# Optimization experiments

Hardware: AMD Instinct MI355X
Metric: run time of the kernel (lower is better)

The kernel has to match this reference:

```python
import jax, jax.numpy as jnp
import numpy as np

N_ENT, N_REL, D, E, NS, B = 100000, 200, 64, 1000000, 4096, 32


def setup_inputs() -> dict:
    key = jax.random.key(0)
    ks = jax.random.split(key, 20)
    s = 1.0 / np.sqrt(D)
    # rotational relation embeddings: [cos|sin ; cos|-sin] -> [2*N_REL, D]
    phases = (2 * np.pi * np.random.RandomState(0).rand(N_REL, D // 2)).astype(np.float32)
    rel = np.concatenate([
        np.concatenate([np.cos(phases), np.sin(phases)], -1),
        np.concatenate([np.cos(phases), -np.sin(phases)], -1)], 0)
    inp = {
        'ent_emb': jax.random.normal(ks[0], (N_ENT, D), jnp.float32) * s,
        'rel_emb': jnp.asarray(rel),
        'gcn_W': jax.random.normal(ks[1], (2, D, D), jnp.float32) * s,
        'gcn_b': jnp.zeros((2, D), jnp.float32),
        'mm_W0': jax.random.normal(ks[2], (3 * D, D), jnp.float32) * s,
        'mm_b0': jnp.zeros((D,), jnp.float32),
        'mm_W1': jax.random.normal(ks[3], (D, D), jnp.float32) * s,
        'mm_b1': jnp.zeros((D,), jnp.float32),
        'mm_Wadv': jax.random.normal(ks[4], (D, 3), jnp.float32) * s,
        'mm_badv': jnp.zeros((3,), jnp.float32),
        'mm_Wval': jax.random.normal(ks[5], (D, 1), jnp.float32) * s,
        'mm_bval': jnp.zeros((1,), jnp.float32),
        'ex_W0': jax.random.normal(ks[6], (D, D), jnp.float32) * s,
        'ex_b0': jnp.zeros((D,), jnp.float32),
        'ex_W1': jax.random.normal(ks[7], (D, D), jnp.float32) * s,
        'ex_b1': jnp.zeros((D,), jnp.float32),
        'ex_Wadv': jax.random.normal(ks[8], (D, 5), jnp.float32) * s,
        'ex_badv': jnp.zeros((5,), jnp.float32),
        'ex_Wval': jax.random.normal(ks[9], (D, 1), jnp.float32) * s,
        'ex_bval': jnp.zeros((1,), jnp.float32),
        'edge_index': jax.random.randint(ks[10], (2, E), 0, N_ENT, jnp.int32),
        'edge_type': jax.random.randint(ks[11], (E,), 0, 2 * N_REL, jnp.int32),
        'short_idx': jax.random.randint(ks[12], (NS,), 0, E, jnp.int32),
        'agent_idx': jax.random.randint(ks[13], (B,), 0, N_ENT, jnp.int32),
    }
    return inp


def _dueling_mlp(h, W0, b0, W1, b1, Wadv, badv, Wval, bval):
    h = jax.nn.relu(h @ W0 + b0)
    h = jax.nn.relu(h @ W1 + b1)
    adv = h @ Wadv + badv
    val = h @ Wval + bval
    return val + adv - adv.mean(-1, keepdims=True)


def reference(ent_emb, rel_emb, gcn_W, gcn_b, mm_W0, mm_b0, mm_W1, mm_b1,
              mm_Wadv, mm_badv, mm_Wval, mm_bval, ex_W0, ex_b0, ex_W1, ex_b1,
              ex_Wadv, ex_badv, ex_Wval, ex_bval,
              edge_index, edge_type, short_idx, agent_idx):
    n = ent_emb.shape[0]
    src, dst = edge_index[0], edge_index[1]
    x = ent_emb
    for l in range(gcn_W.shape[0]):  # GCNConv, normalize=False, no self-loops
        msg = (x @ gcn_W[l])[src]                      # [E, D] gather-transform
        x = jax.ops.segment_sum(msg, dst, num_segments=n) + gcn_b[l]
        x = jax.nn.relu(x)                             # dropout is identity in eval
    # memory-management head: concat(head, relation, tail) for short-term triples
    h_mm = jnp.concatenate([x[src[short_idx]], rel_emb[edge_type[short_idx]],
                            x[dst[short_idx]]], axis=-1)  # [NS, 3D]
    q_mm = _dueling_mlp(h_mm, mm_W0, mm_b0, mm_W1, mm_b1, mm_Wadv, mm_badv, mm_Wval, mm_bval)
    # explore head: agent-node embedding
    q_ex = _dueling_mlp(x[agent_idx], ex_W0, ex_b0, ex_W1, ex_b1, ex_Wadv, ex_badv, ex_Wval, ex_bval)
    return q_mm, q_ex
```

## Files before the change

### kernel.cpp

```cpp
#include <hip/hip_runtime.h>

#define DD 64
#define CAP 32

typedef short bf16x8 __attribute__((ext_vector_type(8)));
typedef float f32x4 __attribute__((ext_vector_type(4)));

static __device__ __forceinline__ unsigned short f2bf(float f) {
  unsigned u = __float_as_uint(f);
  return (unsigned short)((u + 0x7fffu + ((u >> 16) & 1u)) >> 16);
}
static __device__ __forceinline__ unsigned pack2bf(float lo, float hi) {
  return (((unsigned)f2bf(hi)) << 16) | (unsigned)f2bf(lo);
}


__global__ __launch_bounds__(256) void k_zero(
    int* __restrict__ f4, int nf4, int* __restrict__ cnt, int N) {
  const int i = blockIdx.x * 256 + threadIdx.x;
  if (i < nf4) f4[i] = 0;
  if (i < N) cnt[i] = 0;
}

__global__ __launch_bounds__(256) void k_flag2(
    const int* __restrict__ sidx, const int* __restrict__ src,
    const int* __restrict__ dst, const int* __restrict__ aidx,
    unsigned char* __restrict__ flags, int NS, int B) {
  const int i = blockIdx.x * 256 + threadIdx.x;
  if (i < NS) {
    int e = sidx[i];
    flags[src[e]] = 1;
    flags[dst[e]] = 1;
  } else if (i < NS + B) {
    flags[aidx[i - NS]] = 1;
  }
}

__global__ __launch_bounds__(256) void k_flagA(
    const int* __restrict__ src, const int* __restrict__ dst,
    unsigned char* __restrict__ flags, int E) {
  const int e = blockIdx.x * 256 + threadIdx.x;
  if (e < E && (flags[dst[e]] & 1)) {
    int s = src[e];
    flags[s] = flags[s] | 2;
  }
}

__device__ __forceinline__ void gemm_body(
    const float* __restrict__ x, const float* __restrict__ W,
    unsigned short* __restrict__ yh, int N, int bid, int nB) {
  __shared__ unsigned short wt[DD * DD];
  __shared__ float ys[4][16][68];
  for (int i = threadIdx.x; i < DD * DD; i += 256) {
    int k = i >> 6, n = i & 63;
    wt[n * DD + k] = f2bf(W[i]);
  }
  __syncthreads();
  const int wave = threadIdx.x >> 6;
  const int lane = threadIdx.x & 63;
  const int g = lane >> 4;
  const int m = lane & 15;
  bf16x8 bfr[8];
#pragma unroll
  for (int nt = 0; nt < 4; ++nt)
#pragma unroll
    for (int m2 = 0; m2 < 2; ++m2) {
      const int base = (nt * 16 + m) * DD + 4 * g + 32 * m2;
      ushort4 lo = *(const ushort4*)&wt[base];
      ushort4 hi = *(const ushort4*)&wt[base + 16];
      bf16x8 f;
      f[0] = (short)lo.x; f[1] = (short)lo.y; f[2] = (short)lo.z; f[3] = (short)lo.w;
      f[4] = (short)hi.x; f[5] = (short)hi.y; f[6] = (short)hi.z; f[7] = (short)hi.w;
      bfr[nt * 2 + m2] = f;
    }
  const int tiles = (N + 15) / 16;
  for (int t = bid * 4 + wave; t < tiles; t += nB * 4) {
    const int row = t * 16 + m;
    const int rsafe = (row < N) ? row : (N - 1);
    const float* xr = x + (size_t)rsafe * DD + 4 * g;
    float4 a0 = *(const float4*)(xr + 0);
    float4 a1 = *(const float4*)(xr + 16);
    float4 a2 = *(const float4*)(xr + 32);
    float4 a3 = *(const float4*)(xr + 48);
    bf16x8 af0, af1;
    af0[0] = (short)f2bf(a0.x); af0[1] = (short)f2bf(a0.y);
    af0[2] = (short)f2bf(a0.z); af0[3] = (short)f2bf(a0.w);
    af0[4] = (short)f2bf(a1.x); af0[5] = (short)f2bf(a1.y);
    af0[6] = (short)f2bf(a1.z); af0[7] = (short)f2bf(a1.w);
    af1[0] = (short)f2bf(a2.x); af1[1] = (short)f2bf(a2.y);
    af1[2] = (short)f2bf(a2.z); af1[3] = (short)f2bf(a2.w);
    af1[4] = (short)f2bf(a3.x); af1[5] = (short)f2bf(a3.y);
    af1[6] = (short)f2bf(a3.z); af1[7] = (short)f2bf(a3.w);
    f32x4 acc0 = {0.f, 0.f, 0.f, 0.f}, acc1 = acc0, acc2 = acc0, acc3 = acc0;
    acc0 = __builtin_amdgcn_mfma_f32_16x16x32_bf16(af0, bfr[0], acc0, 0, 0, 0);
    acc0 = __builtin_amdgcn_mfma_f32_16x16x32_bf16(af1, bfr[1], acc0, 0, 0, 0);
    acc1 = __builtin_amdgcn_mfma_f32_16x16x32_bf16(af0, bfr[2], acc1, 0, 0, 0);
    acc1 = __builtin_amdgcn_mfma_f32_16x16x32_bf16(af1, bfr[3], acc1, 0, 0, 0);
    acc2 = __builtin_amdgcn_mfma_f32_16x16x32_bf16(af0, bfr[4], acc2, 0, 0, 0);
    acc2 = __builtin_amdgcn_mfma_f32_16x16x32_bf16(af1, bfr[5], acc2, 0, 0, 0);
    acc3 = __builtin_amdgcn_mfma_f32_16x16x32_bf16(af0, bfr[6], acc3, 0, 0, 0);
    acc3 = __builtin_amdgcn_mfma_f32_16x16x32_bf16(af1, bfr[7], acc3, 0, 0, 0);
#pragma unroll
    for (int r = 0; r < 4; ++r) {
      ys[wave][4 * g + r][0 * 16 + m] = acc0[r];
      ys[wave][4 * g + r][1 * 16 + m] = acc1[r];
      ys[wave][4 * g + r][2 * 16 + m] = acc2[r];
      ys[wave][4 * g + r][3 * 16 + m] = acc3[r];
    }
    if (row < N) {
      unsigned short* yr = yh + (size_t)row * DD + g * 16;
      const float* s = &ys[wave][m][g * 16];
      uint4 olo, ohi;
      olo.x = pack2bf(s[0], s[1]);
      olo.y = pack2bf(s[2], s[3]);
      olo.z = pack2bf(s[4], s[5]);
      olo.w = pack2bf(s[6], s[7]);
      ohi.x = pack2bf(s[8], s[9]);
      ohi.y = pack2bf(s[10], s[11]);
      ohi.z = pack2bf(s[12], s[13]);
      ohi.w = pack2bf(s[14], s[15]);
      *(uint4*)yr = olo;
      *(uint4*)(yr + 8) = ohi;
    }
  }
}

__global__ __launch_bounds__(256) void k_pregf(
    const float* __restrict__ x, const float* __restrict__ W,
    unsigned short* __restrict__ yh, int N, int GB,
    const int* __restrict__ src, const int* __restrict__ dst,
    const unsigned char* __restrict__ flags, int* __restrict__ cnt,
    int* __restrict__ csr, int E) {
  const int bid = blockIdx.x;
  if (bid < GB) {
    gemm_body(x, W, yh, N, bid, GB);
  } else {
    int e = (bid - GB) * 256 + threadIdx.x;
    if (e < E) {
      int d = dst[e];
      if (flags[d]) {
        int slot = atomicAdd(&cnt[d], 1);
        if (slot < CAP) csr[d * CAP + slot] = src[e];
      }
    }
  }
}

__global__ __launch_bounds__(256) void k_gemm(
    const float* __restrict__ x, const float* __restrict__ W,
    unsigned short* __restrict__ yh, int N) {
  gemm_body(x, W, yh, N, blockIdx.x, gridDim.x);
}

__global__ __launch_bounds__(256) void k_gather_h(
    const unsigned short* __restrict__ yh, const int* __restrict__ cnt,
    const int* __restrict__ csr, const float* __restrict__ b,
    float* __restrict__ outp, int N, const unsigned char* __restrict__ flags,
    int bit) {
  const int wave = threadIdx.x >> 6;
  const int lane = threadIdx.x & 63;
  const int h = lane >> 5;
  const int c = lane & 31;
  const int n = blockIdx.x * 4 + wave;
  if (n >= N) return;
  if (!(flags[n] & bit)) return;
  const float b0r = b[2 * c];
  const float b1r = b[2 * c + 1];
  int i = n * CAP;
  int c2 = cnt[n];
  c2 = (c2 < CAP) ? c2 : CAP;
  const int end = i + c2;
  float a0 = 0.f, a1 = 0.f;
  for (; i + 8 <= end; i += 8) {
    int ib = __builtin_amdgcn_readfirstlane(i);
    int sA = csr[ib + 0 + h];
    int sB = csr[ib + 2 + h];
    int sC = csr[ib + 4 + h];
    int sD = csr[ib + 6 + h];
    unsigned vA = *(const unsigned*)&yh[(size_t)sA * DD + 2 * c];
    unsigned vB = *(const unsigned*)&yh[(size_t)sB * DD + 2 * c];
    unsigned vC = *(const unsigned*)&yh[(size_t)sC * DD + 2 * c];
    unsigned vD = *(const unsigned*)&yh[(size_t)sD * DD + 2 * c];
    a0 += (__uint_as_float(vA << 16) + __uint_as_float(vB << 16)) +
          (__uint_as_float(vC << 16) + __uint_as_float(vD << 16));
    a1 += (__uint_as_float(vA & 0xffff0000u) + __uint_as_float(vB & 0xffff0000u)) +
          (__uint_as_float(vC & 0xffff0000u) + __uint_as_float(vD & 0xffff0000u));
  }
  for (; i + 2 <= end; i += 2) {
    int sA = csr[__builtin_amdgcn_readfirstlane(i) + h];
    unsigned vA = *(const unsigned*)&yh[(size_t)sA * DD + 2 * c];
    a0 += __uint_as_float(vA << 16);
    a1 += __uint_as_float(vA & 0xffff0000u);
  }
  if (i < end && h == 0) {
    int sA = csr[i];
    unsigned vA = *(const unsigned*)&yh[(size_t)sA * DD + 2 * c];
    a0 += __uint_as_float(vA << 16);
    a1 += __uint_as_float(vA & 0xffff0000u);
  }
  a0 += __shfl_xor(a0, 32);
  a1 += __shfl_xor(a1, 32);
  if (h == 0) {
    float2 r;
    r.x = fmaxf(a0 + b0r, 0.f);
    r.y = fmaxf(a1 + b1r, 0.f);
    *(float2*)&outp[(size_t)n * DD + 2 * c] = r;
  }
}

__global__ __launch_bounds__(256) void k_transform(
    const float* __restrict__ x, const float* __restrict__ W,
    float* __restrict__ y, int n_rows, int relu_in) {
  __shared__ __align__(16) float Ws[DD * DD];
  __shared__ __align__(16) float xs[4][DD];
  for (int i = threadIdx.x; i < DD * DD; i += 256) Ws[i] = W[i];
  __syncthreads();
  const int wave = threadIdx.x >> 6;
  const int lane = threadIdx.x & 63;
  for (int n = blockIdx.x * 4 + wave; n < n_rows; n += gridDim.x * 4) {
    float xv = x[n * DD + lane];
    if (relu_in) xv = fmaxf(xv, 0.f);
    xs[wave][lane] = xv;
    float acc = 0.f;
#pragma unroll
    for (int k4 = 0; k4 < DD / 4; ++k4) {
      float4 h4 = *(const float4*)&xs[wave][k4 * 4];
      acc = fmaf(h4.x, Ws[(k4 * 4 + 0) * DD + lane], acc);
      acc = fmaf(h4.y, Ws[(k4 * 4 + 1) * DD + lane], acc);
      acc = fmaf(h4.z, Ws[(k4 * 4 + 2) * DD + lane], acc);
      acc = fmaf(h4.w, Ws[(k4 * 4 + 3) * DD + lane], acc);
    }
    y[n * DD + lane] = acc;
  }
}

__global__ __launch_bounds__(256) void k_init_bias(
    float4* __restrict__ acc, const float* __restrict__ b, int total4) {
  const float4* b4 = (const float4*)b;
  for (int i = blockIdx.x * blockDim.x + threadIdx.x; i < total4;
       i += gridDim.x * blockDim.x)
    acc[i] = b4[i & 15];
}

__global__ __launch_bounds__(256) void k_scatter(
    const float* __restrict__ y, const int* __restrict__ src,
    const int* __restrict__ dst, float* __restrict__ acc, int E) {
  const int total = E * 16;
  for (int i = blockIdx.x * blockDim.x + threadIdx.x; i < total;
       i += gridDim.x * blockDim.x) {
    int e = i >> 4;
    int d4 = (i & 15) << 2;
    int s = src[e], dd = dst[e];
    float4 v = *(const float4*)&y[s * DD + d4];
    float* ap = &acc[dd * DD + d4];
    unsafeAtomicAdd(ap + 0, v.x);
    unsafeAtomicAdd(ap + 1, v.y);
    unsafeAtomicAdd(ap + 2, v.z);
    unsafeAtomicAdd(ap + 3, v.w);
  }
}

__global__ __launch_bounds__(256) void k_relu_inplace(float* __restrict__ p, int n) {
  for (int i = blockIdx.x * blockDim.x + threadIdx.x; i < n;
       i += gridDim.x * blockDim.x)
    p[i] = fmaxf(p[i], 0.f);
}

__global__ __launch_bounds__(256) void k_mm_head(
    const float* __restrict__ xact, const float* __restrict__ rel,
    const int* __restrict__ src, const int* __restrict__ dst,
    const int* __restrict__ etype, const int* __restrict__ sidx,
    const float* __restrict__ W0, const float* __restrict__ b0,
    const float* __restrict__ W1, const float* __restrict__ b1,
    const float* __restrict__ Wadv, const float* __restrict__ badv,
    const float* __restrict__ Wval, const float* __restrict__ bval,
    float* __restrict__ out, int NS) {
  __shared__ __align__(16) float W0s[192 * DD];
  __shared__ float Wadvs[DD * 3], Wvals[DD], b0s[DD], b1s[DD], badvs[3];
  __shared__ __align__(16) float hs[4][192];
  __shared__ __align__(16) float h1s[4][DD];
  for (int i = threadIdx.x; i < 192 * DD; i += 256) W0s[i] = W0[i];
  for (int i = threadIdx.x; i < DD * 3; i += 256) Wadvs[i] = Wadv[i];
  if (threadIdx.x < DD) {
    Wvals[threadIdx.x] = Wval[threadIdx.x];
    b0s[threadIdx.x] = b0[threadIdx.x];
    b1s[threadIdx.x] = b1[threadIdx.x];
  }
  if (threadIdx.x < 3) badvs[threadIdx.x] = badv[threadIdx.x];
  __syncthreads();
  const float bv = bval[0];
  const int wave = threadIdx.x >> 6;
  const int lane = threadIdx.x & 63;
  for (int i = blockIdx.x * 4 + wave; i < NS; i += gridDim.x * 4) {
    int e = sidx[i];
    int s = src[e], dd = dst[e], t = etype[e];
    hs[wave][lane] = fmaxf(xact[s * DD + lane], 0.f);
    hs[wave][64 + lane] = rel[t * DD + lane];
    hs[wave][128 + lane] = fmaxf(xact[dd * DD + lane], 0.f);
    float acc = b0s[lane];
#pragma unroll
    for (int k4 = 0; k4 < 48; ++k4) {
      float4 h4 = *(const float4*)&hs[wave][k4 * 4];
      acc = fmaf(h4.x, W0s[(k4 * 4 + 0) * DD + lane], acc);
      acc = fmaf(h4.y, W0s[(k4 * 4 + 1) * DD + lane], acc);
      acc = fmaf(h4.z, W0s[(k4 * 4 + 2) * DD + lane], acc);
      acc = fmaf(h4.w, W0s[(k4 * 4 + 3) * DD + lane], acc);
    }
    h1s[wave][lane] = fmaxf(acc, 0.f);
    float acc2 = b1s[lane];
#pragma unroll
    for (int k4 = 0; k4 < 16; ++k4) {
      float4 h4 = *(const float4*)&h1s[wave][k4 * 4];
      acc2 = fmaf(h4.x, W1[(k4 * 4 + 0) * DD + lane], acc2);
      acc2 = fmaf(h4.y, W1[(k4 * 4 + 1) * DD + lane], acc2);
      acc2 = fmaf(h4.z, W1[(k4 * 4 + 2) * DD + lane], acc2);
      acc2 = fmaf(h4.w, W1[(k4 * 4 + 3) * DD + lane], acc2);
    }
    float h2 = fmaxf(acc2, 0.f);
    float p0 = h2 * Wadvs[lane * 3 + 0];
    float p1 = h2 * Wadvs[lane * 3 + 1];
    float p2 = h2 * Wadvs[lane * 3 + 2];
    float pv = h2 * Wvals[lane];
#pragma unroll
    for (int off = 32; off; off >>= 1) {
      p0 += __shfl_xor(p0, off);
      p1 += __shfl_xor(p1, off);
      p2 += __shfl_xor(p2, off);
      pv += __shfl_xor(pv, off);
    }
    if (lane == 0) {
      float a0 = p0 + badvs[0], a1 = p1 + badvs[1], a2 = p2 + badvs[2];
      float val = pv + bv;
      float m = (a0 + a1 + a2) * (1.f / 3.f);
      out[i * 3 + 0] = val + a0 - m;
      out[i * 3 + 1] = val + a1 - m;
      out[i * 3 + 2] = val + a2 - m;
    }
  }
}

__global__ __launch_bounds__(256) void k_ex_head(
    const float* __restrict__ xact, const int* __restrict__ aidx,
    const float* __restrict__ W0, const float* __restrict__ b0,
    const float* __restrict__ W1, const float* __restrict__ b1,
    const float* __restrict__ Wadv, const float* __restrict__ badv,
    const float* __restrict__ Wval, const float* __restrict__ bval,
    float* __restrict__ out, int B) {
  __shared__ __align__(16) float W0s[DD * DD], W1s[DD * DD];
  __shared__ float Wadvs[DD * 5], Wvals[DD], b0s[DD], b1s[DD], badvs[5];
  __shared__ __align__(16) float hs[4][DD], h1s[4][DD];
  for (int i = threadIdx.x; i < DD * DD; i += 256) {
    W0s[i] = W0[i];
    W1s[i] = W1[i];
  }
  for (int i = threadIdx.x; i < DD * 5; i += 256) Wadvs[i] = Wadv[i];
  if (threadIdx.x < DD) {
    Wvals[threadIdx.x] = Wval[threadIdx.x];
    b0s[threadIdx.x] = b0[threadIdx.x];
    b1s[threadIdx.x] = b1[threadIdx.x];
  }
  if (threadIdx.x < 5) badvs[threadIdx.x] = badv[threadIdx.x];
  __syncthreads();
  const float bv = bval[0];
  const int wave = threadIdx.x >> 6;
  const int lane = threadIdx.x & 63;
  const int i = blockIdx.x * 4 + wave;
  if (i >= B) return;
  int n = aidx[i];
  hs[wave][lane] = fmaxf(xact[n * DD + lane], 0.f);
  float acc = b0s[lane];
#pragma unroll
  for (int k4 = 0; k4 < 16; ++k4) {
    float4 h4 = *(const float4*)&hs[wave][k4 * 4];
    acc = fmaf(h4.x, W0s[(k4 * 4 + 0) * DD + lane], acc);
    acc = fmaf(h4.y, W0s[(k4 * 4 + 1) * DD + lane], acc);
    acc = fmaf(h4.z, W0s[(k4 * 4 + 2) * DD + lane], acc);
    acc = fmaf(h4.w, W0s[(k4 * 4 + 3) * DD + lane], acc);
  }
  h1s[wave][lane] = fmaxf(acc, 0.f);
  float acc2 = b1s[lane];
#pragma unroll
  for (int k4 = 0; k4 < 16; ++k4) {
    float4 h4 = *(const float4*)&h1s[wave][k4 * 4];
    acc2 = fmaf(h4.x, W1s[(k4 * 4 + 0) * DD + lane], acc2);
    acc2 = fmaf(h4.y, W1s[(k4 * 4 + 1) * DD + lane], acc2);
    acc2 = fmaf(h4.z, W1s[(k4 * 4 + 2) * DD + lane], acc2);
    acc2 = fmaf(h4.w, W1s[(k4 * 4 + 3) * DD + lane], acc2);
  }
  float h2 = fmaxf(acc2, 0.f);
  float p[6];
#pragma unroll
  for (int c = 0; c < 5; ++c) p[c] = h2 * Wadvs[lane * 5 + c];
  p[5] = h2 * Wvals[lane];
#pragma unroll
  for (int off = 32; off; off >>= 1)
#pragma unroll
    for (int c = 0; c < 6; ++c) p[c] += __shfl_xor(p[c], off);
  if (lane == 0) {
    float a[5];
    float m = 0.f;
#pragma unroll
    for (int c = 0; c < 5; ++c) {
      a[c] = p[c] + badvs[c];
      m += a[c];
    }
    m *= 0.2f;
    float val = p[5] + bv;
#pragma unroll
    for (int c = 0; c < 5; ++c) out[i * 5 + c] = val + a[c] - m;
  }
}

extern "C" void kernel_launch(void* const* d_in, const int* in_sizes, int n_in,
                              void* d_out, int out_size, void* d_ws, size_t ws_size,
                              hipStream_t stream) {
  const float* ent = (const float*)d_in[0];
  const float* rel = (const float*)d_in[1];
  const float* gcnW = (const float*)d_in[2];
  const float* gcnB = (const float*)d_in[3];
  const float* mmW0 = (const float*)d_in[4];
  const float* mmB0 = (const float*)d_in[5];
  const float* mmW1 = (const float*)d_in[6];
  const float* mmB1 = (const float*)d_in[7];
  const float* mmWa = (const float*)d_in[8];
  const float* mmBa = (const float*)d_in[9];
  const float* mmWv = (const float*)d_in[10];
  const float* mmBv = (const float*)d_in[11];
  const float* exW0 = (const float*)d_in[12];
  const float* exB0 = (const float*)d_in[13];
  const float* exW1 = (const float*)d_in[14];
  const float* exB1 = (const float*)d_in[15];
  const float* exWa = (const float*)d_in[16];
  const float* exBa = (const float*)d_in[17];
  const float* exWv = (const float*)d_in[18];
  const float* exBv = (const float*)d_in[19];
  const int* eidx = (const int*)d_in[20];
  const int* etype = (const int*)d_in[21];
  const int* sidx = (const int*)d_in[22];
  const int* aidx = (const int*)d_in[23];

  const int N = in_sizes[0] / DD;
  const int E = in_sizes[20] / 2;
  const int NS = in_sizes[22];
  const int B = in_sizes[23];
  const int* src = eidx;
  const int* dst = eidx + E;

  float* bufA = (float*)d_ws;
  float* bufB = bufA + (size_t)N * DD;
  int* cnt = (int*)(bufB + (size_t)N * DD);
  unsigned char* flags = (unsigned char*)(cnt + N);
  unsigned short* yh = (unsigned short*)bufA;
  int* csr = (int*)d_ws + (size_t)N * DD / 2;
  const int nf4 = (N + 3) / 4;
  const size_t need = ((size_t)2 * N * DD + (size_t)N) * 4 + (size_t)nf4 * 4;

  float* q_mm = (float*)d_out;
  float* q_ex = q_mm + (size_t)NS * 3;

  dim3 blk(256);
  const int eb = (E + 255) / 256;
  const int GB = 512;

  if (ws_size >= need) {
    k_zero<<<(N + 255) / 256, blk, 0, stream>>>((int*)flags, nf4, cnt, N);
    k_flag2<<<(NS + B + 255) / 256, blk, 0, stream>>>(sidx, src, dst, aidx, flags,
                                                      NS, B);
    k_flagA<<<eb, blk, 0, stream>>>(src, dst, flags, E);
    k_pregf<<<GB + eb, blk, 0, stream>>>(ent, gcnW, yh, N, GB, src, dst, flags,
                                         cnt, csr, E);
    k_gather_h<<<(N + 3) / 4, blk, 0, stream>>>(yh, cnt, csr, gcnB, bufB, N, flags,
                                                2);
    k_gemm<<<512, blk, 0, stream>>>(bufB, gcnW + DD * DD, yh, N);
    k_gather_h<<<(N + 3) / 4, blk, 0, stream>>>(yh, cnt, csr, gcnB + DD, bufB, N,
                                                flags, 1);
    k_mm_head<<<256, blk, 0, stream>>>(bufB, rel, src, dst, etype, sidx, mmW0,
                                       mmB0, mmW1, mmB1, mmWa, mmBa, mmWv, mmBv,
                                       q_mm, NS);
    k_ex_head<<<(B + 3) / 4, blk, 0, stream>>>(bufB, aidx, exW0, exB0, exW1, exB1,
                                               exWa, exBa, exWv, exBv, q_ex, B);
  } else {
    k_transform<<<1024, blk, 0, stream>>>(ent, gcnW, bufA, N, 0);
    k_init_bias<<<1024, blk, 0, stream>>>((float4*)bufB, gcnB, N * 16);
    k_scatter<<<2048, blk, 0, stream>>>(bufA, src, dst, bufB, E);
    k_transform<<<1024, blk, 0, stream>>>(bufB, gcnW + DD * DD, bufA, N, 1);
    k_init_bias<<<1024, blk, 0, stream>>>((float4*)bufB, gcnB + DD, N * 16);
    k_scatter<<<2048, blk, 0, stream>>>(bufA, src, dst, bufB, E);
    k_relu_inplace<<<1024, blk, 0, stream>>>(bufB, N * DD);
    k_mm_head<<<256, blk, 0, stream>>>(bufB, rel, src, dst, etype, sidx, mmW0,
                                       mmB0, mmW1, mmB1, mmWa, mmBa, mmWv, mmBv,
                                       q_mm, NS);
    k_ex_head<<<(B + 3) / 4, blk, 0, stream>>>(bufB, aidx, exW0, exB0, exW1, exB1,
                                               exWa, exBa, exWv, exBv, q_ex, B);
  }
}
```

Measured before the change: 133.7 us.

## Fuse layer-1 gather aggregation with layer-2 transform into one kernel

Replaces the separate layer-1 gather kernel and layer-2 GEMM with one kernel. Each wave aggregates a flagged node's neighbours from bf16 features, applies bias and ReLU, then multiplies by W1 held in shared memory and writes bf16 output to a new buffer. This removes the fp32 intermediate round-trip to global memory and one launch, and restricts the transform to flagged nodes. In exchange the workspace grows by another N*D bf16 buffer, and the per-node matvec is done with scalar FMAs that read 16 KB of weights from shared memory.

New measurement: 128.5 us. 1.04x faster.

```diff
diff --git a/kernel.cpp b/kernel.cpp
--- a/kernel.cpp
+++ b/kernel.cpp
@@ -146,10 +146,72 @@
   }
 }
 
-__global__ __launch_bounds__(256) void k_gemm(
-    const float* __restrict__ x, const float* __restrict__ W,
-    unsigned short* __restrict__ yh, int N) {
-  gemm_body(x, W, yh, N, blockIdx.x, gridDim.x);
+__global__ __launch_bounds__(256) void k_g1t(
+    const unsigned short* __restrict__ yh0, const int* __restrict__ cnt,
+    const int* __restrict__ csr, const float* __restrict__ b0,
+    const float* __restrict__ W1, unsigned short* __restrict__ yh1, int N,
+    const unsigned char* __restrict__ flags) {
+  __shared__ __align__(16) float Ws[DD * DD];
+  __shared__ __align__(16) float xs[4][DD];
+  for (int i = threadIdx.x; i < DD * DD; i += 256) Ws[i] = W1[i];
+  __syncthreads();
+  const int wave = threadIdx.x >> 6;
+  const int lane = threadIdx.x & 63;
+  const int h = lane >> 5;
+  const int c = lane & 31;
+  const float b0r = b0[2 * c];
+  const float b1r = b0[2 * c + 1];
+  for (int n = blockIdx.x * 4 + wave; n < N; n += gridDim.x * 4) {
+    if (!(flags[n] & 2)) continue;
+    int i = n * CAP;
+    int c2 = cnt[n];
+    c2 = (c2 < CAP) ? c2 : CAP;
+    const int end = i + c2;
+    float a0 = 0.f, a1 = 0.f;
+    for (; i + 8 <= end; i += 8) {
+      int ib = __builtin_amdgcn_readfirstlane(i);
+      int sA = csr[ib + 0 + h];
+      int sB = csr[ib + 2 + h];
+      int sC = csr[ib + 4 + h];
+      int sD = csr[ib + 6 + h];
+      unsigned vA = *(const unsigned*)&yh0[(size_t)sA * DD + 2 * c];
+      unsigned vB = *(const unsigned*)&yh0[(size_t)sB * DD + 2 * c];
+      unsigned vC = *(const unsigned*)&yh0[(size_t)sC * DD + 2 * c];
+      unsigned vD = *(const unsigned*)&yh0[(size_t)sD * DD + 2 * c];
+      a0 += (__uint_as_float(vA << 16) + __uint_as_float(vB << 16)) +
+            (__uint_as_float(vC << 16) + __uint_as_float(vD << 16));
+      a1 += (__uint_as_float(vA & 0xffff0000u) + __uint_as_float(vB & 0xffff0000u)) +
+            (__uint_as_float(vC & 0xffff0000u) + __uint_as_float(vD & 0xffff0000u));
+    }
+    for (; i + 2 <= end; i += 2) {
+      int sA = csr[__builtin_amdgcn_readfirstlane(i) + h];
+      unsigned vA = *(const unsigned*)&yh0[(size_t)sA * DD + 2 * c];
+      a0 += __uint_as_float(vA << 16);
+      a1 += __uint_as_float(vA & 0xffff0000u);
+    }
+    if (i < end && h == 0) {
+      int sA = csr[i];
+      unsigned vA = *(const unsigned*)&yh0[(size_t)sA * DD + 2 * c];
+      a0 += __uint_as_float(vA << 16);
+      a1 += __uint_as_float(vA & 0xffff0000u);
+    }
+    a0 += __shfl_xor(a0, 32);
+    a1 += __shfl_xor(a1, 32);
+    if (h == 0) {
+      xs[wave][2 * c] = fmaxf(a0 + b0r, 0.f);
+      xs[wave][2 * c + 1] = fmaxf(a1 + b1r, 0.f);
+    }
+    float acc = 0.f;
+#pragma unroll
+    for (int k4 = 0; k4 < 16; ++k4) {
+      float4 h4 = *(const float4*)&xs[wave][k4 * 4];
+      acc = fmaf(h4.x, Ws[(k4 * 4 + 0) * DD + lane], acc);
+      acc = fmaf(h4.y, Ws[(k4 * 4 + 1) * DD + lane], acc);
+      acc = fmaf(h4.z, Ws[(k4 * 4 + 2) * DD + lane], acc);
+      acc = fmaf(h4.w, Ws[(k4 * 4 + 3) * DD + lane], acc);
+    }
+    yh1[(size_t)n * DD + lane] = f2bf(acc);
+  }
 }
 
 __global__ __launch_bounds__(256) void k_gather_h(
@@ -450,10 +512,12 @@
   float* bufB = bufA + (size_t)N * DD;
   int* cnt = (int*)(bufB + (size_t)N * DD);
   unsigned char* flags = (unsigned char*)(cnt + N);
-  unsigned short* yh = (unsigned short*)bufA;
+  const int nf4 = (N + 3) / 4;
+  unsigned short* yh0 = (unsigned short*)bufA;
   int* csr = (int*)d_ws + (size_t)N * DD / 2;
-  const int nf4 = (N + 3) / 4;
-  const size_t need = ((size_t)2 * N * DD + (size_t)N) * 4 + (size_t)nf4 * 4;
+  unsigned short* yh1 = (unsigned short*)((int*)flags + nf4);
+  const size_t need = ((size_t)2 * N * DD + (size_t)N) * 4 + (size_t)nf4 * 4 +
+                      (size_t)N * DD * 2;
 
   float* q_mm = (float*)d_out;
   float* q_ex = q_mm + (size_t)NS * 3;
@@ -467,12 +531,11 @@
     k_flag2<<<(NS + B + 255) / 256, blk, 0, stream>>>(sidx, src, dst, aidx, flags,
                                                       NS, B);
     k_flagA<<<eb, blk, 0, stream>>>(src, dst, flags, E);
-    k_pregf<<<GB + eb, blk, 0, stream>>>(ent, gcnW, yh, N, GB, src, dst, flags,
+    k_pregf<<<GB + eb, blk, 0, stream>>>(ent, gcnW, yh0, N, GB, src, dst, flags,
                                          cnt, csr, E);
-    k_gather_h<<<(N + 3) / 4, blk, 0, stream>>>(yh, cnt, csr, gcnB, bufB, N, flags,
-                                                2);
-    k_gemm<<<512, blk, 0, stream>>>(bufB, gcnW + DD * DD, yh, N);
-    k_gather_h<<<(N + 3) / 4, blk, 0, stream>>>(yh, cnt, csr, gcnB + DD, bufB, N,
+    k_g1t<<<2048, blk, 0, stream>>>(yh0, cnt, csr, gcnB, gcnW + DD * DD, yh1, N,
+                                    flags);
+    k_gather_h<<<(N + 3) / 4, blk, 0, stream>>>(yh1, cnt, csr, gcnB + DD, bufB, N,
                                                 flags, 1);
     k_mm_head<<<256, blk, 0, stream>>>(bufB, rel, src, dst, etype, sidx, mmW0,
                                        mmB0, mmW1, mmB1, mmWa, mmBa, mmWv, mmBv,
```
